# Kernel tuning notes

Measured on AMD Instinct MI355X. Metric: run time of the kernel, lower is better.

Reference implementation:

```python
import jax, jax.numpy as jnp
import numpy as np

K_EDE = 10.0   # self.k
T_EDE = 0.1    # self.t
BN_EPS = 1e-5
T_A = 576.0    # 3*3*64, hardcoded in my_bn1/my_bn2


def qfn(x, prec):
    # dorefa-style round quantizer with straight-through gradient
    n = float(2 ** prec - 1)
    return x + jax.lax.stop_gradient(jnp.round(x * n) / n - x)


@jax.custom_vjp
def binary_quantize(x):
    return jnp.sign(x)


def _bq_fwd(x):
    return jnp.sign(x), x


def _bq_bwd(x, g):
    # IR-Net EDE backward: k * t * (1 - tanh(x*t)^2)
    return (K_EDE * T_EDE * (1.0 - jnp.tanh(x * T_EDE) ** 2) * g,)


binary_quantize.defvjp(_bq_fwd, _bq_bwd)


def _clip_T(x):
    T = jnp.maximum(jnp.abs(x.min()), jnp.abs(x.max()))
    return jax.lax.stop_gradient(jnp.clip(T, 1e-10, 255.0))


def quantize_conv_act(x, prec):
    # my_quantize_conv: clamp to [-T, T], scale to [-1,1], qfn (no rescale by T)
    T = _clip_T(x)
    return qfn(jnp.clip(x, -T, T) / T, prec)


def quantize(x, prec):
    # my_quantize: same but rescaled back by T
    T = _clip_T(x)
    return qfn(jnp.clip(x, -T, T) / T, prec) * T


def ir_conv2d(a, w, stride):
    # IR-Net 1w8a IRConv2d: per-out-channel normalize, binarize (sign), power-of-2 scale
    co = w.shape[0]
    wf = w.reshape(co, -1)
    bw = (w - wf.mean(1)[:, None, None, None]) / jnp.std(wf, axis=1, ddof=1)[:, None, None, None]
    sw = jax.lax.stop_gradient(
        2.0 ** jnp.round(jnp.log2(jnp.abs(bw.reshape(co, -1)).mean(1)))
    )[:, None, None, None]
    bw = binary_quantize(bw) * sw
    return jax.lax.conv_general_dilated(
        a, bw, window_strides=(stride, stride), padding=[(1, 1), (1, 1)],
        dimension_numbers=('NCHW', 'OIHW', 'NCHW'))


def bn_as_quantized_affine(x, gamma, beta, mean, var):
    # my_bn1/my_bn2 (eval mode): BN folded into per-channel scale+bias.
    # The original builds a CxC diagonal 1x1 conv; since off-diagonal entries are 0,
    # both the quantization stats (max|.|) and the conv reduce exactly to this
    # per-channel affine, which is the faithful fused form.
    std = jnp.sqrt(var + BN_EPS)
    w = gamma / std
    b = beta - w * mean
    qw = quantize(w, 3)
    qb = quantize(b, 12)
    aq = qfn(x / T_A, 10) * T_A  # my_quantize_activation(input, 10, T_a)
    return aq * qw[None, :, None, None] + qb[None, :, None, None]


def _block(x, w1, w2, g1, b1, m1, v1, g2, b2, m2, v2):
    xq = quantize_conv_act(x, 3)
    out = ir_conv2d(xq, w1, 1)
    out = bn_as_quantized_affine(out, g1, b1, m1, v1) + xq  # identity shortcut
    out = jnp.clip(out, -1.0, 1.0)  # hardtanh
    x1 = quantize_conv_act(out, 3)
    out = ir_conv2d(x1, w2, 1)
    out = bn_as_quantized_affine(out, g2, b2, m2, v2) + x1
    return jnp.clip(out, -1.0, 1.0)


def setup_inputs() -> dict:
    key = jax.random.key(0)
    ks = jax.random.split(key, 11)
    B, C, H, W = 128, 64, 56, 56
    return {
        'x': jax.random.normal(ks[0], (B, C, H, W), jnp.float32),
        'w1': jax.random.normal(ks[1], (C, C, 3, 3), jnp.float32) * 0.1,
        'w2': jax.random.normal(ks[2], (C, C, 3, 3), jnp.float32) * 0.1,
        'g1': jax.random.uniform(ks[3], (C,), jnp.float32, 0.5, 1.5),
        'b1': jax.random.normal(ks[4], (C,), jnp.float32) * 0.1,
        'm1': jax.random.normal(ks[5], (C,), jnp.float32) * 0.1,
        'v1': jax.random.uniform(ks[6], (C,), jnp.float32, 0.5, 1.5),
        'g2': jax.random.uniform(ks[7], (C,), jnp.float32, 0.5, 1.5),
        'b2': jax.random.normal(ks[8], (C,), jnp.float32) * 0.1,
        'm2': jax.random.normal(ks[9], (C,), jnp.float32) * 0.1,
        'v2': jax.random.uniform(ks[10], (C,), jnp.float32, 0.5, 1.5),
    }


def reference(x, w1, w2, g1, b1, m1, v1, g2, b2, m2, v2):
    return _block(x, w1, w2, g1, b1, m1, v1, g2, b2, m2, v2)
```

## Files before the change

### kernel.cpp

```cpp
#include <hip/hip_runtime.h>
#include <stdint.h>

typedef int v4i   __attribute__((ext_vector_type(4)));
typedef int v16i  __attribute__((ext_vector_type(16)));

#define B_    128
#define C_    64
#define H_    56
#define W_    56
#define HW_   3136
#define NELEM (B_*C_*HW_)

#define OFF_K0   0
#define OFF_K1   ((size_t)NELEM)
#define OFF_WB   ((size_t)2*NELEM)
#define OFF_PAR  (OFF_WB + 2*4*9*64*16)
#define OFF_MAX  (OFF_PAR + 384*4)

__device__ __forceinline__ float pw_reduce64(float r) {
    r = __fadd_rn(r, __shfl_xor(r, 1, 64));
    r = __fadd_rn(r, __shfl_xor(r, 2, 64));
    r = __fadd_rn(r, __shfl_xor(r, 4, 64));
    r = __fadd_rn(r, __shfl_xor(r, 8, 64));
    r = __fadd_rn(r, __shfl_xor(r, 16, 64));
    r = __fadd_rn(r, __shfl_xor(r, 32, 64));
    return r;
}

__global__ void k_pre(const float* __restrict__ x, unsigned* __restrict__ maxbits,
                      const float* __restrict__ w1, const float* __restrict__ w2,
                      int8_t* __restrict__ wb, float* __restrict__ par,
                      const float* __restrict__ g1, const float* __restrict__ bb1,
                      const float* __restrict__ mm1, const float* __restrict__ vv1,
                      const float* __restrict__ g2, const float* __restrict__ bb2,
                      const float* __restrict__ mm2, const float* __restrict__ vv2) {
    __shared__ float smax[4];
    const int b = blockIdx.x;
    const int tid = threadIdx.x;
    if (b < 1024) {
        float m = 0.f;
        const int n4 = NELEM / 4;
        for (int i = b * 256 + tid; i < n4; i += 1024 * 256) {
            float4 v = ((const float4*)x)[i];
            m = fmaxf(m, fmaxf(fmaxf(fabsf(v.x), fabsf(v.y)), fmaxf(fabsf(v.z), fabsf(v.w))));
        }
        for (int off = 32; off; off >>= 1) m = fmaxf(m, __shfl_down(m, off, 64));
        if ((tid & 63) == 0) smax[tid >> 6] = m;
        __syncthreads();
        if (tid == 0) {
            float mm = fmaxf(fmaxf(smax[0], smax[1]), fmaxf(smax[2], smax[3]));
            atomicMax(maxbits, __float_as_uint(mm));
        }
    } else if (b < 1056) {
        const int idx = (b - 1024) * 4 + (tid >> 6);
        const int layer = idx >> 6, co = idx & 63;
        const int lane = tid & 63;
        const float* w = (layer ? w2 : w1) + (size_t)co * 576;
        const int base = (lane >> 3) * 72 + (lane & 7);

        float v[9];
#pragma unroll
        for (int i = 0; i < 9; i++) v[i] = w[base + 8 * i];

        float s = v[0];
#pragma unroll
        for (int i = 1; i < 9; i++) s = __fadd_rn(s, v[i]);
        const float mean = __fdiv_rn(pw_reduce64(s), 576.0f);

        float d0 = __fsub_rn(v[0], mean);
        float sq = __fmul_rn(d0, d0);
#pragma unroll
        for (int i = 1; i < 9; i++) {
            float d = __fsub_rn(v[i], mean);
            sq = __fadd_rn(sq, __fmul_rn(d, d));
        }
        const float sig = __fsqrt_rn(__fdiv_rn(pw_reduce64(sq), 575.0f));

        float sa = fabsf(__fdiv_rn(__fsub_rn(v[0], mean), sig));
#pragma unroll
        for (int i = 1; i < 9; i++)
            sa = __fadd_rn(sa, fabsf(__fdiv_rn(__fsub_rn(v[i], mean), sig)));
        const float ma = __fdiv_rn(pw_reduce64(sa), 576.0f);
        const float p  = rintf(log2f(ma));
        if (lane == 0) par[256 + layer * 64 + co] = __fdiv_rn(exp2f(p), 7.0f);

#pragma unroll
        for (int i = 0; i < 9; i++) {
            int ig = base + 8 * i;
            float d = __fsub_rn(v[i], mean);
            int8_t sg = (d > 0.0f) ? (int8_t)1 : ((d < 0.0f) ? (int8_t)-1 : (int8_t)0);
            int ci = ig / 9, tp = ig % 9;
            wb[((((size_t)layer * 4 + (ci >> 4)) * 9 + tp) * 64 + co) * 16 + (ci & 15)] = sg;
        }
    } else {
        if (tid < 128) {
            const int layer = tid >> 6;
            const int c = tid & 63;
            const float* g  = layer ? g2  : g1;
            const float* be = layer ? bb2 : bb1;
            const float* mu = layer ? mm2 : mm1;
            const float* va = layer ? vv2 : vv1;
            const float stdv = __fsqrt_rn(__fadd_rn(va[c], 1e-5f));
            const float w = __fdiv_rn(g[c], stdv);
            const float bb = __fsub_rn(be[c], __fmul_rn(w, mu[c]));
            float aw = fabsf(w), ab = fabsf(bb);
            for (int off = 32; off; off >>= 1) {
                aw = fmaxf(aw, __shfl_xor(aw, off, 64));
                ab = fmaxf(ab, __shfl_xor(ab, off, 64));
            }
            const float Tw = fminf(fmaxf(aw, 1e-10f), 255.0f);
            const float Tb = fminf(fmaxf(ab, 1e-10f), 255.0f);
            {
                float vq = __fdiv_rn(fminf(fmaxf(w, -Tw), Tw), Tw);
                float r  = rintf(__fmul_rn(vq, 7.0f));
                float qf = __fadd_rn(vq, __fsub_rn(__fdiv_rn(r, 7.0f), vq));
                par[layer * 64 + c] = __fmul_rn(qf, Tw);
            }
            {
                float vq = __fdiv_rn(fminf(fmaxf(bb, -Tb), Tb), Tb);
                float r  = rintf(__fmul_rn(vq, 4095.0f));
                float qf = __fadd_rn(vq, __fsub_rn(__fdiv_rn(r, 4095.0f), vq));
                par[128 + layer * 64 + c] = __fmul_rn(qf, Tb);
            }
        }
    }
}

__global__ void k_quant(const float* __restrict__ x, const unsigned* __restrict__ maxbits,
                        int8_t* __restrict__ k8) {
    __shared__ unsigned tile[56 * 17];
    const int n = blockIdx.x / H_;
    const int y = blockIdx.x % H_;
    const float T = fminf(fmaxf(__uint_as_float(*maxbits), 1e-10f), 255.0f);
    const double dinv = 1.0 / (double)T;
    const int t = threadIdx.x;
    if (t < 224) {
        const int cb = t / 14, xb = t % 14;
        const float* src = x + ((size_t)(n * 64 + 4 * cb)) * HW_ + y * 56 + 4 * xb;
        int kq[4][4];
#pragma unroll
        for (int i = 0; i < 4; i++) {
            float4 v = *(const float4*)(src + (size_t)i * HW_);
            const float e[4] = {v.x, v.y, v.z, v.w};
#pragma unroll
            for (int j = 0; j < 4; j++) {
                const float tc = fminf(fmaxf(e[j], -T), T);
                const float u  = (float)((double)tc * dinv);
                kq[i][j] = (int)rintf(__fmul_rn(u, 7.0f));
            }
        }
#pragma unroll
        for (int j = 0; j < 4; j++) {
            const unsigned d = (kq[0][j] & 255) | ((kq[1][j] & 255) << 8) |
                               ((kq[2][j] & 255) << 16) | ((unsigned)(kq[3][j] & 255) << 24);
            tile[(4 * xb + j) * 17 + cb] = d;
        }
    }
    __syncthreads();
    unsigned* dst = (unsigned*)(k8 + ((size_t)(n * 56 + y)) * 56 * 64);
    for (int u = t; u < 896; u += 256)
        dst[u] = tile[(u >> 4) * 17 + (u & 15)];
}

template <int LAYER>
__global__ __launch_bounds__(448, 2) void k_conv(const int8_t* __restrict__ kin,
                                                 const int8_t* __restrict__ wb,
                                                 const float* __restrict__ par,
                                                 int8_t* __restrict__ kout,
                                                 float* __restrict__ fout) {
    __shared__ __align__(16) int8_t halo[4 * 6 * 58 * 16];
    __shared__ __align__(16) int8_t wsm[4 * 9 * 64 * 16];
    const int n  = blockIdx.x / 14;
    const int y0 = (blockIdx.x % 14) * 4;
    const int tid = threadIdx.x;

    for (int u = tid; u < 1392; u += 448) {
        const int q = u & 3, v = u >> 2;
        const int r = v / 58, xp = v % 58;
        const int y = y0 - 1 + r, xg = xp - 1;
        int4 val = {0, 0, 0, 0};
        if (y >= 0 && y < 56 && xg >= 0 && xg < 56)
            val = *(const int4*)(kin + (((size_t)(n * 56 + y)) * 56 + xg) * 64 + q * 16);
        *(int4*)(halo + (((q * 6 + r) * 58 + xp) << 4)) = val;
    }
    const int8_t* wsrc = wb + (size_t)(LAYER - 1) * (4 * 9 * 64 * 16);
    for (int u = tid; u < 2304; u += 448)
        *(int4*)(wsm + u * 16) = *(const int4*)(wsrc + u * 16);
    __syncthreads();

    const int wv = tid >> 6, lane = tid & 63;
    const int mbase = wv * 32;
    const int ml = lane & 31;
    const int khalf = lane >> 5;
    const int m = mbase + ml;
    const int rm = m / 56, cm = m % 56;

    v16i acc0, acc1;
#pragma unroll
    for (int i = 0; i < 16; i++) { acc0[i] = 0; acc1[i] = 0; }

#pragma unroll
    for (int s = 0; s < 9; s++) {
        const int ky = s / 3, kx = s % 3;
#pragma unroll
        for (int kb = 0; kb < 2; kb++) {
            const int q = khalf + 2 * kb;
            v4i a  = *(const v4i*)(halo + ((((q * 6 + rm + ky) * 58) + cm + kx) << 4));
            v4i b0 = *(const v4i*)(wsm  + (((q * 9 + s) * 64 + ml) << 4));
            v4i b1 = *(const v4i*)(wsm  + (((q * 9 + s) * 64 + 32 + ml) << 4));
            acc0 = __builtin_amdgcn_mfma_i32_32x32x32_i8(a, b0, acc0, 0, 0, 0);
            acc1 = __builtin_amdgcn_mfma_i32_32x32x32_i8(a, b1, acc1, 0, 0, 0);
        }
    }

    const float* qw = par + (LAYER - 1) * 64;
    const float* qb = par + 128 + (LAYER - 1) * 64;
    const float* sc = par + 256 + (LAYER - 1) * 64;
#pragma unroll
    for (int g = 0; g < 4; g++) {
        const int mb = mbase + 8 * g + 4 * khalf;
        const int rloc = mb / 56;
        const int cl0  = mb % 56;
#pragma unroll
        for (int t = 0; t < 2; t++) {
            const int co = ml + t * 32;
            const float qwf = qw[co], qbf = qb[co], scf = sc[co];
            const int qc = co >> 4, cl = co & 15;
            const int clw = cl & ~3, cb8 = (cl & 3) * 8;
            const int pixbase = (qc * 6 + rloc + 1) * 58 + cl0 + 1;
            float vals[4];
#pragma unroll
            for (int i = 0; i < 4; i++) {
                const int   S  = t ? acc1[4 * g + i] : acc0[4 * g + i];
                const float Sf = (float)S;
                const float convf = __fmul_rn(Sf, scf);
                const float xb = (float)((double)convf * (1.0 / 576.0));
                const float rr = rintf(__fmul_rn(xb, 1023.0f));
                const float q1 = (float)((double)rr * (1.0 / 1023.0));
                const float y1 = __fadd_rn(xb, __fsub_rn(q1, xb));
                const float aq = __fmul_rn(y1, 576.0f);
                const unsigned wd = *(const unsigned*)(halo + ((pixbase + i) << 4) + clw);
                const int   kc = (int)(int8_t)(wd >> cb8);
                const float xqv = (float)((double)kc * (1.0 / 7.0));
                float val = __fadd_rn(__fadd_rn(__fmul_rn(aq, qwf), qbf), xqv);
                val = fminf(fmaxf(val, -1.0f), 1.0f);
                if (LAYER == 1) {
                    const int k2 = (int)rintf(__fmul_rn(val, 7.0f));
                    kout[(((size_t)(n * 56 + y0 + rloc)) * 56 + cl0 + i) * 64 + co] = (int8_t)k2;
                } else {
                    vals[i] = val;
                }
            }
            if (LAYER == 2) {
                float4 o = make_float4(vals[0], vals[1], vals[2], vals[3]);
                *(float4*)(fout + ((size_t)(n * 64 + co)) * HW_ + (y0 + rloc) * 56 + cl0) = o;
            }
        }
    }
}

extern "C" void kernel_launch(void* const* d_in, const int* in_sizes, int n_in,
                              void* d_out, int out_size, void* d_ws, size_t ws_size,
                              hipStream_t stream) {
    const float* x  = (const float*)d_in[0];
    const float* w1 = (const float*)d_in[1];
    const float* w2 = (const float*)d_in[2];
    const float* g1 = (const float*)d_in[3];
    const float* b1 = (const float*)d_in[4];
    const float* m1 = (const float*)d_in[5];
    const float* v1 = (const float*)d_in[6];
    const float* g2 = (const float*)d_in[7];
    const float* b2 = (const float*)d_in[8];
    const float* m2 = (const float*)d_in[9];
    const float* v2 = (const float*)d_in[10];

    char* ws = (char*)d_ws;
    int8_t*  k0  = (int8_t*)(ws + OFF_K0);
    int8_t*  k1  = (int8_t*)(ws + OFF_K1);
    int8_t*  wbp = (int8_t*)(ws + OFF_WB);
    float*   par = (float*)(ws + OFF_PAR);
    unsigned* mx = (unsigned*)(ws + OFF_MAX);

    hipMemsetAsync(mx, 0, 4, stream);
    k_pre<<<1057, 256, 0, stream>>>(x, mx, w1, w2, wbp, par,
                                    g1, b1, m1, v1, g2, b2, m2, v2);
    k_quant<<<B_ * H_, 256, 0, stream>>>(x, mx, k0);
    k_conv<1><<<B_ * 14, 448, 0, stream>>>(k0, wbp, par, k1, nullptr);
    k_conv<2><<<B_ * 14, 448, 0, stream>>>(k1, wbp, par, nullptr, (float*)d_out);
}
```

Before: 315.7 us.

## Fuse both binary conv layers into one row-streaming kernel with LDS ring buffers

Replaces the two separate conv kernels with a single kernel in which each block handles half an image. The block streams 4-row strips through an 8-slot LDS ring for the quantized input and the intermediate activation. Layer-2 convolution runs one strip behind layer 1, so the int8 intermediate never goes to global memory, and the next input rows are prefetched into registers during compute. This removes the intermediate tensor round trip and one launch. In exchange, grid parallelism drops sharply, LDS use per block grows, and the strips are serialized with block-wide syncs.

```diff
diff --git a/kernel.cpp b/kernel.cpp
--- a/kernel.cpp
+++ b/kernel.cpp
@@ -162,100 +162,192 @@
         dst[u] = tile[(u >> 4) * 17 + (u & 15)];
 }
 
-template <int LAYER>
-__global__ __launch_bounds__(448, 2) void k_conv(const int8_t* __restrict__ kin,
-                                                 const int8_t* __restrict__ wb,
-                                                 const float* __restrict__ par,
-                                                 int8_t* __restrict__ kout,
-                                                 float* __restrict__ fout) {
-    __shared__ __align__(16) int8_t halo[4 * 6 * 58 * 16];
-    __shared__ __align__(16) int8_t wsm[4 * 9 * 64 * 16];
-    const int n  = blockIdx.x / 14;
-    const int y0 = (blockIdx.x % 14) * 4;
+#define EPI_CHAIN(S_, scf_, kc_, qwf_, qbf_, OUT_)                          \
+    {   const float Sf_ = (float)(S_);                                      \
+        const float convf_ = __fmul_rn(Sf_, scf_);                          \
+        const float xb_ = (float)((double)convf_ * (1.0 / 576.0));          \
+        const float rr_ = rintf(__fmul_rn(xb_, 1023.0f));                   \
+        const float q1_ = (float)((double)rr_ * (1.0 / 1023.0));            \
+        const float y1_ = __fadd_rn(xb_, __fsub_rn(q1_, xb_));              \
+        const float aq_ = __fmul_rn(y1_, 576.0f);                           \
+        const float xqv_ = (float)((double)(kc_) * (1.0 / 7.0));            \
+        float vv_ = __fadd_rn(__fadd_rn(__fmul_rn(aq_, qwf_), qbf_), xqv_); \
+        OUT_ = fminf(fmaxf(vv_, -1.0f), 1.0f); }
+
+__global__ __launch_bounds__(448, 2) void k_fused(const int8_t* __restrict__ k0,
+                                                  const int8_t* __restrict__ wb,
+                                                  const float* __restrict__ par,
+                                                  float* __restrict__ fout) {
+    __shared__ __align__(16) int8_t wsm[2 * 4 * 9 * 64 * 16];
+    __shared__ __align__(16) int8_t k0b[4 * 8 * 58 * 16];
+    __shared__ __align__(16) int8_t x1b[4 * 8 * 58 * 16];
+    const int n = blockIdx.x >> 1;
+    const int b = (blockIdx.x & 1) * 28;
     const int tid = threadIdx.x;
-
-    for (int u = tid; u < 1392; u += 448) {
-        const int q = u & 3, v = u >> 2;
-        const int r = v / 58, xp = v % 58;
-        const int y = y0 - 1 + r, xg = xp - 1;
-        int4 val = {0, 0, 0, 0};
-        if (y >= 0 && y < 56 && xg >= 0 && xg < 56)
-            val = *(const int4*)(kin + (((size_t)(n * 56 + y)) * 56 + xg) * 64 + q * 16);
-        *(int4*)(halo + (((q * 6 + r) * 58 + xp) << 4)) = val;
-    }
-    const int8_t* wsrc = wb + (size_t)(LAYER - 1) * (4 * 9 * 64 * 16);
-    for (int u = tid; u < 2304; u += 448)
-        *(int4*)(wsm + u * 16) = *(const int4*)(wsrc + u * 16);
-    __syncthreads();
-
     const int wv = tid >> 6, lane = tid & 63;
     const int mbase = wv * 32;
     const int ml = lane & 31;
     const int khalf = lane >> 5;
     const int m = mbase + ml;
-    const int rm = m / 56, cm = m % 56;
-
-    v16i acc0, acc1;
-#pragma unroll
-    for (int i = 0; i < 16; i++) { acc0[i] = 0; acc1[i] = 0; }
-
-#pragma unroll
-    for (int s = 0; s < 9; s++) {
-        const int ky = s / 3, kx = s % 3;
-#pragma unroll
-        for (int kb = 0; kb < 2; kb++) {
-            const int q = khalf + 2 * kb;
-            v4i a  = *(const v4i*)(halo + ((((q * 6 + rm + ky) * 58) + cm + kx) << 4));
-            v4i b0 = *(const v4i*)(wsm  + (((q * 9 + s) * 64 + ml) << 4));
-            v4i b1 = *(const v4i*)(wsm  + (((q * 9 + s) * 64 + 32 + ml) << 4));
-            acc0 = __builtin_amdgcn_mfma_i32_32x32x32_i8(a, b0, acc0, 0, 0, 0);
-            acc1 = __builtin_amdgcn_mfma_i32_32x32x32_i8(a, b1, acc1, 0, 0, 0);
-        }
-    }
-
-    const float* qw = par + (LAYER - 1) * 64;
-    const float* qb = par + 128 + (LAYER - 1) * 64;
-    const float* sc = par + 256 + (LAYER - 1) * 64;
-#pragma unroll
-    for (int g = 0; g < 4; g++) {
-        const int mb = mbase + 8 * g + 4 * khalf;
-        const int rloc = mb / 56;
-        const int cl0  = mb % 56;
-#pragma unroll
-        for (int t = 0; t < 2; t++) {
-            const int co = ml + t * 32;
-            const float qwf = qw[co], qbf = qb[co], scf = sc[co];
-            const int qc = co >> 4, cl = co & 15;
-            const int clw = cl & ~3, cb8 = (cl & 3) * 8;
-            const int pixbase = (qc * 6 + rloc + 1) * 58 + cl0 + 1;
-            float vals[4];
-#pragma unroll
-            for (int i = 0; i < 4; i++) {
-                const int   S  = t ? acc1[4 * g + i] : acc0[4 * g + i];
-                const float Sf = (float)S;
-                const float convf = __fmul_rn(Sf, scf);
-                const float xb = (float)((double)convf * (1.0 / 576.0));
-                const float rr = rintf(__fmul_rn(xb, 1023.0f));
-                const float q1 = (float)((double)rr * (1.0 / 1023.0));
-                const float y1 = __fadd_rn(xb, __fsub_rn(q1, xb));
-                const float aq = __fmul_rn(y1, 576.0f);
-                const unsigned wd = *(const unsigned*)(halo + ((pixbase + i) << 4) + clw);
-                const int   kc = (int)(int8_t)(wd >> cb8);
-                const float xqv = (float)((double)kc * (1.0 / 7.0));
-                float val = __fadd_rn(__fadd_rn(__fmul_rn(aq, qwf), qbf), xqv);
-                val = fminf(fmaxf(val, -1.0f), 1.0f);
-                if (LAYER == 1) {
-                    const int k2 = (int)rintf(__fmul_rn(val, 7.0f));
-                    kout[(((size_t)(n * 56 + y0 + rloc)) * 56 + cl0 + i) * 64 + co] = (int8_t)k2;
-                } else {
-                    vals[i] = val;
-                }
-            }
-            if (LAYER == 2) {
-                float4 o = make_float4(vals[0], vals[1], vals[2], vals[3]);
-                *(float4*)(fout + ((size_t)(n * 64 + co)) * HW_ + (y0 + rloc) * 56 + cl0) = o;
-            }
-        }
+    const int ym = m / 56, cm = m % 56;
+
+    for (int u = tid; u < 4608; u += 448)
+        *(int4*)(wsm + u * 16) = *(const int4*)(wb + (size_t)u * 16);
+    for (int u = tid; u < 1392; u += 448) {
+        const int q = u & 3, vv = u >> 2;
+        const int rr = vv / 58, xp = vv % 58;
+        const int r = b - 2 + rr, xg = xp - 1;
+        int4 val = {0, 0, 0, 0};
+        if (r >= 0 && r < 56 && xg >= 0 && xg < 56)
+            val = *(const int4*)(k0 + (((size_t)(n * 56 + r)) * 56 + xg) * 64 + q * 16);
+        *(int4*)(k0b + (((q * 8 + ((r + 2) & 7)) * 58 + xp) << 4)) = val;
+    }
+    if (tid < 64) {
+        const int q = tid & 3, slot = (tid >> 2) & 7, xs = (tid >> 5) & 1;
+        *(int4*)(x1b + (((q * 8 + slot) * 58 + xs * 57) << 4)) = (int4){0, 0, 0, 0};
+    }
+    __syncthreads();
+
+    const float* qw1 = par;       const float* qw2 = par + 64;
+    const float* qb1 = par + 128; const float* qb2 = par + 192;
+    const float* sc1 = par + 256; const float* sc2 = par + 320;
+
+    int4 pre[3];
+#pragma unroll 1
+    for (int i = 0; i < 8; ++i) {
+        if (i < 7) {
+            const int R0 = b + 4 * i + 4;
+#pragma unroll
+            for (int it = 0; it < 3; ++it) {
+                const int u = tid + it * 448;
+                int4 val = {0, 0, 0, 0};
+                if (u < 928) {
+                    const int q = u & 3, vv = u >> 2;
+                    const int rr = vv / 58, xp = vv % 58;
+                    const int r = R0 + rr, xg = xp - 1;
+                    if (r >= 0 && r < 56 && xg >= 0 && xg < 56)
+                        val = *(const int4*)(k0 + (((size_t)(n * 56 + r)) * 56 + xg) * 64 + q * 16);
+                }
+                pre[it] = val;
+            }
+        }
+        const int y1base = b - 1 + 4 * i;
+        {
+            v16i acc0, acc1;
+#pragma unroll
+            for (int z = 0; z < 16; z++) { acc0[z] = 0; acc1[z] = 0; }
+#pragma unroll
+            for (int s = 0; s < 9; s++) {
+                const int ky = s / 3, kx = s % 3;
+                const int arow = y1base + ym + ky - 1;
+                const int aslot = (arow + 2) & 7;
+#pragma unroll
+                for (int kb = 0; kb < 2; kb++) {
+                    const int q = khalf + 2 * kb;
+                    v4i a  = *(const v4i*)(k0b + (((q * 8 + aslot) * 58 + cm + kx) << 4));
+                    v4i b0 = *(const v4i*)(wsm + (((q * 9 + s) * 64 + ml) << 4));
+                    v4i b1 = *(const v4i*)(wsm + (((q * 9 + s) * 64 + 32 + ml) << 4));
+                    acc0 = __builtin_amdgcn_mfma_i32_32x32x32_i8(a, b0, acc0, 0, 0, 0);
+                    acc1 = __builtin_amdgcn_mfma_i32_32x32x32_i8(a, b1, acc1, 0, 0, 0);
+                }
+            }
+            const int bsh = (ml & 3) * 8;
+#pragma unroll
+            for (int t = 0; t < 2; t++) {
+                const int co = ml + t * 32;
+                const float qwf = qw1[co], qbf = qb1[co], scf = sc1[co];
+                const int qc = co >> 4, cl = co & 15;
+                const int clw = cl & ~3, cb8 = (cl & 3) * 8;
+#pragma unroll
+                for (int g = 0; g < 4; g++) {
+                    const int mb = mbase + 8 * g + 4 * khalf;
+                    const int rl = mb / 56, c0 = mb % 56;
+                    const int y1g = y1base + rl;
+                    const bool vrow = (y1g >= 0) && (y1g <= 55);
+                    const bool wen  = (y1g <= b + 28);
+                    const int ksl = (y1g + 2) & 7;
+                    const int xsl = (y1g + 1) & 7;
+                    const int resb = (qc * 8 + ksl) * 58 + c0 + 1;
+                    const int outb = (qc * 8 + xsl) * 58 + c0 + 1;
+#pragma unroll
+                    for (int i4 = 0; i4 < 4; i4++) {
+                        const int S = t ? acc1[4 * g + i4] : acc0[4 * g + i4];
+                        const unsigned wd = *(const unsigned*)(k0b + ((resb + i4) << 4) + clw);
+                        const int kc = (int)(int8_t)(wd >> cb8);
+                        float val; EPI_CHAIN(S, scf, kc, qwf, qbf, val);
+                        int k2 = (int)rintf(__fmul_rn(val, 7.0f));
+                        if (!vrow) k2 = 0;
+                        unsigned vp = ((unsigned)(k2 & 255)) << bsh;
+                        vp |= (unsigned)__shfl_xor((int)vp, 1, 64);
+                        vp |= (unsigned)__shfl_xor((int)vp, 2, 64);
+                        if (wen && (ml & 3) == 0)
+                            *(unsigned*)(x1b + ((outb + i4) << 4) + clw) = vp;
+                    }
+                }
+            }
+        }
+        __syncthreads();
+
+        if (i < 7) {
+            const int R0 = b + 4 * i + 4;
+#pragma unroll
+            for (int it = 0; it < 3; ++it) {
+                const int u = tid + it * 448;
+                if (u < 928) {
+                    const int q = u & 3, vv = u >> 2;
+                    const int rr = vv / 58, xp = vv % 58;
+                    const int r = R0 + rr;
+                    *(int4*)(k0b + (((q * 8 + ((r + 2) & 7)) * 58 + xp) << 4)) = pre[it];
+                }
+            }
+        }
+        if (i >= 1) {
+            const int y2base = b + 4 * (i - 1);
+            v16i acc0, acc1;
+#pragma unroll
+            for (int z = 0; z < 16; z++) { acc0[z] = 0; acc1[z] = 0; }
+#pragma unroll
+            for (int s = 0; s < 9; s++) {
+                const int ky = s / 3, kx = s % 3;
+                const int arow = y2base + ym + ky - 1;
+                const int aslot = (arow + 1) & 7;
+#pragma unroll
+                for (int kb = 0; kb < 2; kb++) {
+                    const int q = khalf + 2 * kb;
+                    v4i a  = *(const v4i*)(x1b + (((q * 8 + aslot) * 58 + cm + kx) << 4));
+                    v4i b0 = *(const v4i*)(wsm + 36864 + (((q * 9 + s) * 64 + ml) << 4));
+                    v4i b1 = *(const v4i*)(wsm + 36864 + (((q * 9 + s) * 64 + 32 + ml) << 4));
+                    acc0 = __builtin_amdgcn_mfma_i32_32x32x32_i8(a, b0, acc0, 0, 0, 0);
+                    acc1 = __builtin_amdgcn_mfma_i32_32x32x32_i8(a, b1, acc1, 0, 0, 0);
+                }
+            }
+#pragma unroll
+            for (int t = 0; t < 2; t++) {
+                const int co = ml + t * 32;
+                const float qwf = qw2[co], qbf = qb2[co], scf = sc2[co];
+                const int qc = co >> 4, cl = co & 15;
+                const int clw = cl & ~3, cb8 = (cl & 3) * 8;
+#pragma unroll
+                for (int g = 0; g < 4; g++) {
+                    const int mb = mbase + 8 * g + 4 * khalf;
+                    const int rl = mb / 56, c0 = mb % 56;
+                    const int y2g = y2base + rl;
+                    const int xsl = (y2g + 1) & 7;
+                    const int resb = (qc * 8 + xsl) * 58 + c0 + 1;
+                    float vals[4];
+#pragma unroll
+                    for (int i4 = 0; i4 < 4; i4++) {
+                        const int S = t ? acc1[4 * g + i4] : acc0[4 * g + i4];
+                        const unsigned wd = *(const unsigned*)(x1b + ((resb + i4) << 4) + clw);
+                        const int kc = (int)(int8_t)(wd >> cb8);
+                        EPI_CHAIN(S, scf, kc, qwf, qbf, vals[i4]);
+                    }
+                    float4 o = make_float4(vals[0], vals[1], vals[2], vals[3]);
+                    *(float4*)(fout + ((size_t)(n * 64 + co)) * HW_ + y2g * 56 + c0) = o;
+                }
+            }
+        }
+        if (i < 7) __syncthreads();
     }
 }
 
@@ -276,7 +368,6 @@
 
     char* ws = (char*)d_ws;
     int8_t*  k0  = (int8_t*)(ws + OFF_K0);
-    int8_t*  k1  = (int8_t*)(ws + OFF_K1);
     int8_t*  wbp = (int8_t*)(ws + OFF_WB);
     float*   par = (float*)(ws + OFF_PAR);
     unsigned* mx = (unsigned*)(ws + OFF_MAX);
@@ -285,6 +376,5 @@
     k_pre<<<1057, 256, 0, stream>>>(x, mx, w1, w2, wbp, par,
                                     g1, b1, m1, v1, g2, b2, m2, v2);
     k_quant<<<B_ * H_, 256, 0, stream>>>(x, mx, k0);
-    k_conv<1><<<B_ * 14, 448, 0, stream>>>(k0, wbp, par, k1, nullptr);
-    k_conv<2><<<B_ * 14, 448, 0, stream>>>(k1, wbp, par, nullptr, (float*)d_out);
-}
+    k_fused<<<B_ * 2, 448, 0, stream>>>(k0, wbp, par, (float*)d_out);
+}
```

Measured after the change: 313.9 us. No clear change (-0.6%).
